# Optimization experiments

Measured on AMD Instinct MI355X. Metric: run time of the kernel, lower is better.

The kernel has to match this reference:

```python
import jax, jax.numpy as jnp
import numpy as np
import math

B, S, D, H = 2, 4096, 512, 8
HD = D // H

def setup_inputs() -> dict:
    key = jax.random.key(0)
    ks = jax.random.split(key, 12)
    s = 0.02
    return {
        "query": jax.random.normal(ks[0], (B, S, D), jnp.float32),
        "key": jax.random.normal(ks[1], (B, S, D), jnp.float32),
        "value": jax.random.normal(ks[2], (B, S, D), jnp.float32),
        "mask": jnp.ones((B, S, S), dtype=bool),
        "Wq": jax.random.normal(ks[3], (D, D), jnp.float32) * s,
        "bq": jnp.zeros((D,), jnp.float32),
        "Wk": jax.random.normal(ks[4], (D, D), jnp.float32) * s,
        "bk": jnp.zeros((D,), jnp.float32),
        "Wv": jax.random.normal(ks[5], (D, D), jnp.float32) * s,
        "bv": jnp.zeros((D,), jnp.float32),
        "Wo": jax.random.normal(ks[6], (D, D), jnp.float32) * s,
        "bo": jnp.zeros((D,), jnp.float32),
    }

def reference(query, key, value, mask, Wq, bq, Wk, bk, Wv, bv, Wo, bo):
    # projections (torch Linear: x @ W.T + b)
    q = query @ Wq.T + bq   # [B,S,D]
    k = key @ Wk.T + bk
    v = value @ Wv.T + bv
    # split heads -> [B,H,S,hd]
    q = q.reshape(B, S, H, HD).transpose(0, 2, 1, 3)
    k = k.reshape(B, S, H, HD).transpose(0, 2, 1, 3)
    v = v.reshape(B, S, H, HD).transpose(0, 2, 1, 3)
    score = jnp.einsum('bhqd,bhkd->bhqk', q, k) / math.sqrt(HD)
    score = jnp.where(mask[:, None, :, :], score, -jnp.inf)
    weight = jax.nn.softmax(score, axis=-1)
    out = jnp.einsum('bhqk,bhkd->bhqd', weight, v)
    out = out.transpose(0, 2, 1, 3).reshape(B, S, D)
    return out @ Wo.T + bo
```

## Files before the change

### kernel.cpp

```cpp
#include <hip/hip_runtime.h>


typedef short s16x8 __attribute__((ext_vector_type(8)));
typedef float f32x4 __attribute__((ext_vector_type(4)));
typedef float f32x16 __attribute__((ext_vector_type(16)));
typedef unsigned u32x4 __attribute__((ext_vector_type(4)));

#define MFMA_BF16_16(a, b, c) __builtin_amdgcn_mfma_f32_16x16x32_bf16((a), (b), (c), 0, 0, 0)
#define MFMA_BF16_32(a, b, c) __builtin_amdgcn_mfma_f32_32x32x16_bf16((a), (b), (c), 0, 0, 0)

#if __has_builtin(__builtin_amdgcn_exp2f)
#define EXP2F __builtin_amdgcn_exp2f
#else
#define EXP2F exp2f
#endif

__device__ __forceinline__ unsigned short f2bf(float f) {
  unsigned u = __float_as_uint(f);
  u += 0x7FFFu + ((u >> 16) & 1u);
  return (unsigned short)(u >> 16);
}

__device__ __forceinline__ float bf2f(unsigned short u) {
  return __uint_as_float((unsigned)u << 16);
}

__device__ __forceinline__ unsigned cvt_pk_bf16(float lo, float hi) {
  unsigned r;
  asm("v_cvt_pk_bf16_f32 %0, %1, %2" : "=v"(r) : "v"(lo), "v"(hi));
  return r;
}

__device__ __forceinline__ void pl_swap(unsigned& a, unsigned& b) {
#if __has_builtin(__builtin_amdgcn_permlane32_swap)
  auto r = __builtin_amdgcn_permlane32_swap(a, b, false, false);
  a = r[0];
  b = r[1];
#else
  asm volatile("v_permlane32_swap_b32 %0, %1" : "+v"(a), "+v"(b));
#endif
}

__device__ __forceinline__ float partner_sum(float x) {
  unsigned a = __float_as_uint(x), b = a;
  pl_swap(a, b);
  return __uint_as_float(a) + __uint_as_float(b);
}

__device__ __forceinline__ float exp_block(f32x16& sc) {
#pragma unroll
  for (int r = 0; r < 16; ++r) sc[r] = EXP2F(sc[r]);
  const float a = (sc[0] + sc[1]) + (sc[2] + sc[3]);
  const float b = (sc[4] + sc[5]) + (sc[6] + sc[7]);
  const float c = (sc[8] + sc[9]) + (sc[10] + sc[11]);
  const float d = (sc[12] + sc[13]) + (sc[14] + sc[15]);
  return (a + b) + (c + d);
}

__device__ __forceinline__ ushort4 cvt4(float4 v) {
  ushort4 b;
  b.x = f2bf(v.x); b.y = f2bf(v.y); b.z = f2bf(v.z); b.w = f2bf(v.w);
  return b;
}

__global__ __launch_bounds__(256, 3) void gemm_qkv(const float* __restrict__ Aq,
                                                   const float* __restrict__ Ak,
                                                   const float* __restrict__ Av,
                                                   const float* __restrict__ Wq,
                                                   const float* __restrict__ Wk,
                                                   const float* __restrict__ Wv,
                                                   const float* __restrict__ bq,
                                                   const float* __restrict__ bk,
                                                   const float* __restrict__ bv,
                                                   unsigned short* __restrict__ oq,
                                                   unsigned short* __restrict__ ok,
                                                   unsigned short* __restrict__ ov,
                                                   float qscale) {
  constexpr int KD = 512;
  __shared__ unsigned short As[128][72];
  __shared__ unsigned short Bs[128][72];

  const int bid = blockIdx.x;
  const int wg = (bid & 7) * 96 + (bid >> 3);
  const int n0 = (wg & 3) * 128;
  const int mseg = wg >> 2;
  const int seg = mseg >> 6;
  const int m0 = (mseg & 63) * 128;

  const float* A = (seg == 0) ? Aq : (seg == 1) ? Ak : Av;
  const float* W = (seg == 0) ? Wq : (seg == 1) ? Wk : Wv;
  const float* bias = (seg == 0) ? bq : (seg == 1) ? bk : bv;
  unsigned short* outb = (seg == 0) ? oq : (seg == 1) ? ok : ov;
  const float scale = (seg == 0) ? qscale : 1.0f;

  const int t = threadIdx.x;
  const int lane = t & 63;
  const int w = t >> 6;
  const int wr = w >> 1, wc = w & 1;
  const int x = lane & 15, g = lane >> 4;

  const f32x4 ZERO = {0.f, 0.f, 0.f, 0.f};
  f32x4 acc[4][4];
#pragma unroll
  for (int i = 0; i < 4; ++i)
#pragma unroll
    for (int j = 0; j < 4; ++j) acc[i][j] = ZERO;

  const int r0 = t >> 4, c4 = t & 15;

  float4 av[8];
#pragma unroll
  for (int i = 0; i < 8; ++i)
    av[i] = *(const float4*)(A + (size_t)(m0 + r0 + 16 * i) * KD + c4 * 4);

  for (int kt = 0; kt < KD / 64; ++kt) {
    const int k0 = kt * 64;
    if (kt) __syncthreads();
    float4 wtmp[8];
#pragma unroll
    for (int i = 0; i < 8; ++i)
      wtmp[i] = *(const float4*)(W + (size_t)(n0 + r0 + 16 * i) * KD + k0 + c4 * 4);
#pragma unroll
    for (int i = 0; i < 8; ++i)
      *(ushort4*)(&As[r0 + 16 * i][c4 * 4]) = cvt4(av[i]);
#pragma unroll
    for (int i = 0; i < 8; ++i)
      *(ushort4*)(&Bs[r0 + 16 * i][c4 * 4]) = cvt4(wtmp[i]);
    if (kt < 7) {
#pragma unroll
      for (int i = 0; i < 8; ++i)
        av[i] = *(const float4*)(A + (size_t)(m0 + r0 + 16 * i) * KD + k0 + 64 + c4 * 4);
    }
    __syncthreads();
#pragma unroll
    for (int ks = 0; ks < 2; ++ks) {
      s16x8 af[4], bfq[4];
#pragma unroll
      for (int mt = 0; mt < 4; ++mt)
        af[mt] = *(const s16x8*)(&As[wr * 64 + mt * 16 + x][ks * 32 + g * 8]);
#pragma unroll
      for (int nt = 0; nt < 4; ++nt)
        bfq[nt] = *(const s16x8*)(&Bs[wc * 64 + nt * 16 + x][ks * 32 + g * 8]);
#pragma unroll
      for (int mt = 0; mt < 4; ++mt)
#pragma unroll
        for (int nt = 0; nt < 4; ++nt)
          acc[mt][nt] = MFMA_BF16_16(af[mt], bfq[nt], acc[mt][nt]);
    }
  }

#pragma unroll
  for (int mt = 0; mt < 4; ++mt) {
#pragma unroll
    for (int nt = 0; nt < 4; ++nt) {
      const int n = n0 + wc * 64 + nt * 16 + x;
      const float bv2 = bias[n];
      const int h = n >> 6, hd = n & 63;
#pragma unroll
      for (int r = 0; r < 4; ++r) {
        const int m = m0 + wr * 64 + mt * 16 + g * 4 + r;
        const float val = (acc[mt][nt][r] + bv2) * scale;
        const int b = m >> 12, s = m & 4095;
        size_t off;
        if (seg < 2)
          off = ((size_t)(b * 8 + h) * 4096 + s) * 64 + hd;
        else
          off = ((size_t)(b * 8 + h) * 64 + hd) * 4096 + s;
        outb[off] = f2bf(val);
      }
    }
  }
}

__global__ __launch_bounds__(256, 3) void gemm_o(const unsigned short* __restrict__ o0,
                                                 const unsigned short* __restrict__ o1,
                                                 const float* __restrict__ l0,
                                                 const float* __restrict__ l1,
                                                 const float* __restrict__ W,
                                                 const float* __restrict__ bias,
                                                 float* __restrict__ out) {
  constexpr int KD = 512;
  __shared__ unsigned short As[64][72];
  __shared__ unsigned short Bs[128][72];

  const int bid = blockIdx.x;
  const int wg = (bid & 7) * 64 + (bid >> 3);
  const int n0 = (wg & 3) * 128;
  const int m0 = (wg >> 2) * 64;

  const int t = threadIdx.x;
  const int lane = t & 63;
  const int w = t >> 6;
  const int wr = w >> 1, wc = w & 1;
  const int x = lane & 15, g = lane >> 4;

  const f32x4 ZERO = {0.f, 0.f, 0.f, 0.f};
  f32x4 acc[2][4];
#pragma unroll
  for (int i = 0; i < 2; ++i)
#pragma unroll
    for (int j = 0; j < 4; ++j) acc[i][j] = ZERO;

  const int r0 = t >> 4, c4 = t & 15;

  int rowi[2], segi[2], bi[2], si[2];
  s16x8 pa[2], pb[2];
  float l0v[2], l1v[2];
#pragma unroll
  for (int i = 0; i < 2; ++i) {
    const int c = t + 256 * i;
    rowi[i] = c >> 3;
    segi[i] = c & 7;
    const int m = m0 + rowi[i];
    bi[i] = m >> 12;
    si[i] = m & 4095;
    const size_t ao = (size_t)m * 512 + segi[i] * 8;
    pa[i] = *(const s16x8*)(o0 + ao);
    pb[i] = *(const s16x8*)(o1 + ao);
    l0v[i] = l0[(size_t)(bi[i] * 8 + 0) * 4096 + si[i]];
    l1v[i] = l1[(size_t)(bi[i] * 8 + 0) * 4096 + si[i]];
  }

  for (int kt = 0; kt < KD / 64; ++kt) {
    const int k0 = kt * 64;
    if (kt) __syncthreads();
    float4 wtmp[8];
#pragma unroll
    for (int i = 0; i < 8; ++i)
      wtmp[i] = *(const float4*)(W + (size_t)(n0 + r0 + 16 * i) * KD + k0 + c4 * 4);
#pragma unroll
    for (int i = 0; i < 2; ++i) {
      const float inv = 1.0f / (l0v[i] + l1v[i]);
      const s16x8 A0 = pa[i], A1 = pb[i];
      unsigned q0_ = cvt_pk_bf16((bf2f(A0[0]) + bf2f(A1[0])) * inv,
                                 (bf2f(A0[1]) + bf2f(A1[1])) * inv);
      unsigned q1_ = cvt_pk_bf16((bf2f(A0[2]) + bf2f(A1[2])) * inv,
                                 (bf2f(A0[3]) + bf2f(A1[3])) * inv);
      unsigned q2_ = cvt_pk_bf16((bf2f(A0[4]) + bf2f(A1[4])) * inv,
                                 (bf2f(A0[5]) + bf2f(A1[5])) * inv);
      unsigned q3_ = cvt_pk_bf16((bf2f(A0[6]) + bf2f(A1[6])) * inv,
                                 (bf2f(A0[7]) + bf2f(A1[7])) * inv);
      u32x4 fu = {q0_, q1_, q2_, q3_};
      *(s16x8*)(&As[rowi[i]][segi[i] * 8]) = __builtin_bit_cast(s16x8, fu);
    }
#pragma unroll
    for (int i = 0; i < 8; ++i)
      *(ushort4*)(&Bs[r0 + 16 * i][c4 * 4]) = cvt4(wtmp[i]);
    if (kt < 7) {
      const int h = kt + 1;
#pragma unroll
      for (int i = 0; i < 2; ++i) {
        const size_t ao = (size_t)(m0 + rowi[i]) * 512 + h * 64 + segi[i] * 8;
        pa[i] = *(const s16x8*)(o0 + ao);
        pb[i] = *(const s16x8*)(o1 + ao);
        l0v[i] = l0[(size_t)(bi[i] * 8 + h) * 4096 + si[i]];
        l1v[i] = l1[(size_t)(bi[i] * 8 + h) * 4096 + si[i]];
      }
    }
    __syncthreads();
#pragma unroll
    for (int ks = 0; ks < 2; ++ks) {
      s16x8 af[2], bfq[4];
#pragma unroll
      for (int mt = 0; mt < 2; ++mt)
        af[mt] = *(const s16x8*)(&As[wr * 32 + mt * 16 + x][ks * 32 + g * 8]);
#pragma unroll
      for (int nt = 0; nt < 4; ++nt)
        bfq[nt] = *(const s16x8*)(&Bs[wc * 64 + nt * 16 + x][ks * 32 + g * 8]);
#pragma unroll
      for (int mt = 0; mt < 2; ++mt)
#pragma unroll
        for (int nt = 0; nt < 4; ++nt)
          acc[mt][nt] = MFMA_BF16_16(af[mt], bfq[nt], acc[mt][nt]);
    }
  }

#pragma unroll
  for (int mt = 0; mt < 2; ++mt) {
#pragma unroll
    for (int nt = 0; nt < 4; ++nt) {
      const int n = n0 + wc * 64 + nt * 16 + x;
      const float bv = bias[n];
#pragma unroll
      for (int r = 0; r < 4; ++r) {
        const int m = m0 + wr * 32 + mt * 16 + g * 4 + r;
        out[(size_t)m * 512 + n] = acc[mt][nt][r] + bv;
      }
    }
  }
}

__global__ __launch_bounds__(512, 2) void attn_fwd(const unsigned short* __restrict__ Qw,
                                                   const unsigned short* __restrict__ Kw,
                                                   const unsigned short* __restrict__ Vw,
                                                   unsigned short* __restrict__ Op,
                                                   float* __restrict__ Lp) {
  constexpr int S = 4096;
  constexpr int NP = 16;
  __shared__ unsigned short SM[8][64][72];

  const int t = threadIdx.x;
  const int lane = t & 63;
  const int w = t >> 6;
  const int q = lane & 31;
  const int hi = lane >> 5;

  const int bid = blockIdx.x;
  const int xcd = bid & 7;
  const int slot = bid >> 3;
  const int bh = xcd * 2 + (slot & 1);
  const int rest = slot >> 1;
  const int chunk = rest >> 4;
  const int qx = rest & 15;
  const int q0 = qx * 256 + w * 32;

  const unsigned short* Qb = Qw + (size_t)bh * S * 64;
  const unsigned short* Kb = Kw + (size_t)bh * S * 64 + (size_t)chunk * 2048 * 64;
  const unsigned short* Vb = Vw + (size_t)bh * 64 * S + chunk * 2048;

  s16x8 qf[4];
#pragma unroll
  for (int ks = 0; ks < 4; ++ks)
    qf[ks] = *(const s16x8*)(Qb + (size_t)(q0 + q) * 64 + ks * 16 + hi * 8);

  const f32x16 NEG8 = -8.0f;
  f32x16 ot0 = 0.f, ot1 = 0.f;
  float l_loc = 0.f;

  const int strow = t >> 3, stseg = t & 7;
  const unsigned short* kp = Kb + (size_t)strow * 64 + stseg * 8;
  const unsigned short* vp = Vb + (size_t)strow * S + stseg * 8;

  *(s16x8*)(&SM[0][strow][stseg * 8]) = *(const s16x8*)(kp);
  *(s16x8*)(&SM[1][strow][stseg * 8]) = *(const s16x8*)(kp + 4096);
  *(s16x8*)(&SM[4][strow][stseg * 8]) = *(const s16x8*)(vp);
  *(s16x8*)(&SM[5][strow][stseg * 8]) = *(const s16x8*)(vp + 64);
  s16x8 krA = *(const s16x8*)(kp + 2 * 4096);
  s16x8 krB = *(const s16x8*)(kp + 3 * 4096);
  s16x8 vrA = *(const s16x8*)(vp + 128);
  s16x8 vrB = *(const s16x8*)(vp + 192);
  __syncthreads();

  f32x16 sc0 = NEG8, sc1 = NEG8, sc2 = NEG8, sc3 = NEG8;

  __builtin_amdgcn_s_setprio(1);
#pragma unroll
  for (int ks = 0; ks < 4; ++ks) {
    const int col = ks * 16 + hi * 8;
    s16x8 a00 = *(const s16x8*)(&SM[0][q][col]);
    s16x8 a01 = *(const s16x8*)(&SM[0][32 + q][col]);
    s16x8 a10 = *(const s16x8*)(&SM[1][q][col]);
    s16x8 a11 = *(const s16x8*)(&SM[1][32 + q][col]);
    sc0 = MFMA_BF16_32(a00, qf[ks], sc0);
    sc1 = MFMA_BF16_32(a01, qf[ks], sc1);
    sc2 = MFMA_BF16_32(a10, qf[ks], sc2);
    sc3 = MFMA_BF16_32(a11, qf[ks], sc3);
  }
  __builtin_amdgcn_s_setprio(0);

  for (int p = 0; p < NP; ++p) {
    const int cb = (p & 1) * 2;
    const int nb = ((p + 1) & 1) * 2;

    if (p + 1 < NP) {
      *(s16x8*)(&SM[nb][strow][stseg * 8]) = krA;
      *(s16x8*)(&SM[nb + 1][strow][stseg * 8]) = krB;
      *(s16x8*)(&SM[4 + nb][strow][stseg * 8]) = vrA;
      *(s16x8*)(&SM[5 + nb][strow][stseg * 8]) = vrB;
    }
    if (p + 2 < NP) {
      krA = *(const s16x8*)(kp + (size_t)(2 * p + 4) * 4096);
      krB = *(const s16x8*)(kp + (size_t)(2 * p + 5) * 4096);
      vrA = *(const s16x8*)(vp + (2 * p + 4) * 64);
      vrB = *(const s16x8*)(vp + (2 * p + 5) * 64);
    }

    l_loc += exp_block(sc0);
    l_loc += exp_block(sc1);
    l_loc += exp_block(sc2);
    l_loc += exp_block(sc3);

#define PV_HALF(SC, VB, CBASE)                                                \
    _Pragma("unroll")                                                         \
    for (int cc = 0; cc < 2; ++cc) {                                          \
      const int b0 = cc * 8;                                                  \
      unsigned w0 = cvt_pk_bf16(SC[b0 + 0], SC[b0 + 1]);                      \
      unsigned w1 = cvt_pk_bf16(SC[b0 + 2], SC[b0 + 3]);                      \
      unsigned w2 = cvt_pk_bf16(SC[b0 + 4], SC[b0 + 5]);                      \
      unsigned w3 = cvt_pk_bf16(SC[b0 + 6], SC[b0 + 7]);                      \
      pl_swap(w0, w2);                                                        \
      pl_swap(w1, w3);                                                        \
      u32x4 fu = {w0, w1, w2, w3};                                            \
      const s16x8 pf = __builtin_bit_cast(s16x8, fu);                         \
      const int col = (CBASE + cc) * 16 + hi * 8;                             \
      __builtin_amdgcn_s_setprio(1);                                          \
      {                                                                       \
        s16x8 a0 = *(const s16x8*)(&SM[VB][q][col]);                          \
        s16x8 a1 = *(const s16x8*)(&SM[VB][32 + q][col]);                     \
        ot0 = MFMA_BF16_32(a0, pf, ot0);                                      \
        ot1 = MFMA_BF16_32(a1, pf, ot1);                                      \
      }                                                                       \
      __builtin_amdgcn_s_setprio(0);                                          \
    }

    PV_HALF(sc0, 4 + cb, 0)
    PV_HALF(sc1, 4 + cb, 2)
    PV_HALF(sc2, 5 + cb, 0)
    PV_HALF(sc3, 5 + cb, 2)
#undef PV_HALF

    __syncthreads();

    if (p + 1 < NP) {
      sc0 = NEG8; sc1 = NEG8; sc2 = NEG8; sc3 = NEG8;
      __builtin_amdgcn_s_setprio(1);
#pragma unroll
      for (int ks = 0; ks < 4; ++ks) {
        const int col = ks * 16 + hi * 8;
        s16x8 a00 = *(const s16x8*)(&SM[nb][q][col]);
        s16x8 a01 = *(const s16x8*)(&SM[nb][32 + q][col]);
        s16x8 a10 = *(const s16x8*)(&SM[nb + 1][q][col]);
        s16x8 a11 = *(const s16x8*)(&SM[nb + 1][32 + q][col]);
        sc0 = MFMA_BF16_32(a00, qf[ks], sc0);
        sc1 = MFMA_BF16_32(a01, qf[ks], sc1);
        sc2 = MFMA_BF16_32(a10, qf[ks], sc2);
        sc3 = MFMA_BF16_32(a11, qf[ks], sc3);
      }
      __builtin_amdgcn_s_setprio(0);
    }
  }

  unsigned short* EP = &SM[0][0][0];
  const int erow = w * 32 + q;
#pragma unroll
  for (int c = 0; c < 4; ++c) {
    const int d = 8 * c + 4 * hi;
    *(unsigned*)(EP + erow * 72 + d) = cvt_pk_bf16(ot0[4 * c + 0], ot0[4 * c + 1]);
    *(unsigned*)(EP + erow * 72 + d + 2) = cvt_pk_bf16(ot0[4 * c + 2], ot0[4 * c + 3]);
    *(unsigned*)(EP + erow * 72 + 32 + d) = cvt_pk_bf16(ot1[4 * c + 0], ot1[4 * c + 1]);
    *(unsigned*)(EP + erow * 72 + 32 + d + 2) = cvt_pk_bf16(ot1[4 * c + 2], ot1[4 * c + 3]);
  }
  const float lf = partner_sum(l_loc);
  if (hi == 0)
    Lp[((size_t)chunk * 16 + bh) * 4096 + q0 + q] = lf;

  const int bb = bh >> 3, h = bh & 7;
  unsigned short* Ob = Op + (size_t)chunk * 8192 * 512;
#pragma unroll
  for (int i = 0; i < 4; ++i) {
    const int r = i * 8 + (lane >> 3), sg = lane & 7;
    s16x8 vrow = *(const s16x8*)(EP + (w * 32 + r) * 72 + sg * 8);
    *(s16x8*)(Ob + ((size_t)(bb * 4096 + q0 + r)) * 512 + h * 64 + sg * 8) = vrow;
  }
}

extern "C" void kernel_launch(void* const* d_in, const int* in_sizes, int n_in,
                              void* d_out, int out_size, void* d_ws, size_t ws_size,
                              hipStream_t stream) {
  const float* query = (const float*)d_in[0];
  const float* keyin = (const float*)d_in[1];
  const float* value = (const float*)d_in[2];
  const float* Wq = (const float*)d_in[4];
  const float* bq = (const float*)d_in[5];
  const float* Wk = (const float*)d_in[6];
  const float* bk = (const float*)d_in[7];
  const float* Wv = (const float*)d_in[8];
  const float* bv = (const float*)d_in[9];
  const float* Wo = (const float*)d_in[10];
  const float* bo = (const float*)d_in[11];
  float* out = (float*)d_out;

  unsigned short* qws = (unsigned short*)d_ws;
  unsigned short* kws = qws + (size_t)8192 * 512;
  unsigned short* vws = kws + (size_t)8192 * 512;
  unsigned short* opart = vws + (size_t)8192 * 512;
  float* lpart = (float*)(opart + (size_t)2 * 8192 * 512);

  const float qscale = 0.125f * 1.44269504f;
  gemm_qkv<<<768, 256, 0, stream>>>(query, keyin, value, Wq, Wk, Wv,
                                    bq, bk, bv, qws, kws, vws, qscale);
  attn_fwd<<<512, 512, 0, stream>>>(qws, kws, vws, opart, lpart);
  gemm_o<<<512, 256, 0, stream>>>(opart, opart + (size_t)8192 * 512,
                                  lpart, lpart + (size_t)16 * 4096,
                                  Wo, bo, out);
}
```

Measured before the change: 137.9 us.

## Restructure attention to 4 waves with 64 query rows each and 64-key tiles

The attention kernel drops from 8 to 4 waves per block, and each wave now owns 64 query rows in two 32-row groups. Each K/V fragment read from shared memory therefore feeds twice as many MFMAs, which cuts LDS traffic per FLOP. The key loop now steps through 32 tiles of 64 keys with a smaller double buffer, and the cross-iteration QK prefetch is gone. Separately, the GEMM kernels replace the software bf16 rounding with the packed hardware convert. The cost is higher register pressure (more accumulators and Q fragments), and fewer waves are left to hide latency.

```diff
diff --git a/kernel.cpp b/kernel.cpp
--- a/kernel.cpp
+++ b/kernel.cpp
@@ -5,6 +5,7 @@
 typedef float f32x4 __attribute__((ext_vector_type(4)));
 typedef float f32x16 __attribute__((ext_vector_type(16)));
 typedef unsigned u32x4 __attribute__((ext_vector_type(4)));
+typedef unsigned u32x2 __attribute__((ext_vector_type(2)));
 
 #define MFMA_BF16_16(a, b, c) __builtin_amdgcn_mfma_f32_16x16x32_bf16((a), (b), (c), 0, 0, 0)
 #define MFMA_BF16_32(a, b, c) __builtin_amdgcn_mfma_f32_32x32x16_bf16((a), (b), (c), 0, 0, 0)
@@ -15,12 +16,6 @@
 #define EXP2F exp2f
 #endif
 
-__device__ __forceinline__ unsigned short f2bf(float f) {
-  unsigned u = __float_as_uint(f);
-  u += 0x7FFFu + ((u >> 16) & 1u);
-  return (unsigned short)(u >> 16);
-}
-
 __device__ __forceinline__ float bf2f(unsigned short u) {
   return __uint_as_float((unsigned)u << 16);
 }
@@ -28,6 +23,11 @@
 __device__ __forceinline__ unsigned cvt_pk_bf16(float lo, float hi) {
   unsigned r;
   asm("v_cvt_pk_bf16_f32 %0, %1, %2" : "=v"(r) : "v"(lo), "v"(hi));
+  return r;
+}
+
+__device__ __forceinline__ u32x2 cvt4pk(float4 v) {
+  u32x2 r = {cvt_pk_bf16(v.x, v.y), cvt_pk_bf16(v.z, v.w)};
   return r;
 }
 
@@ -57,10 +57,16 @@
   return (a + b) + (c + d);
 }
 
-__device__ __forceinline__ ushort4 cvt4(float4 v) {
-  ushort4 b;
-  b.x = f2bf(v.x); b.y = f2bf(v.y); b.z = f2bf(v.z); b.w = f2bf(v.w);
-  return b;
+__device__ __forceinline__ s16x8 make_pf(float s0, float s1, float s2, float s3,
+                                         float s4, float s5, float s6, float s7) {
+  unsigned w0 = cvt_pk_bf16(s0, s1);
+  unsigned w1 = cvt_pk_bf16(s2, s3);
+  unsigned w2 = cvt_pk_bf16(s4, s5);
+  unsigned w3 = cvt_pk_bf16(s6, s7);
+  pl_swap(w0, w2);
+  pl_swap(w1, w3);
+  u32x4 fu = {w0, w1, w2, w3};
+  return __builtin_bit_cast(s16x8, fu);
 }
 
 __global__ __launch_bounds__(256, 3) void gemm_qkv(const float* __restrict__ Aq,
@@ -122,10 +128,10 @@
       wtmp[i] = *(const float4*)(W + (size_t)(n0 + r0 + 16 * i) * KD + k0 + c4 * 4);
 #pragma unroll
     for (int i = 0; i < 8; ++i)
-      *(ushort4*)(&As[r0 + 16 * i][c4 * 4]) = cvt4(av[i]);
+      *(u32x2*)(&As[r0 + 16 * i][c4 * 4]) = cvt4pk(av[i]);
 #pragma unroll
     for (int i = 0; i < 8; ++i)
-      *(ushort4*)(&Bs[r0 + 16 * i][c4 * 4]) = cvt4(wtmp[i]);
+      *(u32x2*)(&Bs[r0 + 16 * i][c4 * 4]) = cvt4pk(wtmp[i]);
     if (kt < 7) {
 #pragma unroll
       for (int i = 0; i < 8; ++i)
@@ -166,7 +172,8 @@
           off = ((size_t)(b * 8 + h) * 4096 + s) * 64 + hd;
         else
           off = ((size_t)(b * 8 + h) * 64 + hd) * 4096 + s;
-        outb[off] = f2bf(val);
+        const unsigned short bf = (unsigned short)(cvt_pk_bf16(val, val) & 0xffffu);
+        outb[off] = bf;
       }
     }
   }
@@ -245,7 +252,7 @@
     }
 #pragma unroll
     for (int i = 0; i < 8; ++i)
-      *(ushort4*)(&Bs[r0 + 16 * i][c4 * 4]) = cvt4(wtmp[i]);
+      *(u32x2*)(&Bs[r0 + 16 * i][c4 * 4]) = cvt4pk(wtmp[i]);
     if (kt < 7) {
       const int h = kt + 1;
 #pragma unroll
@@ -290,14 +297,14 @@
   }
 }
 
-__global__ __launch_bounds__(512, 2) void attn_fwd(const unsigned short* __restrict__ Qw,
+__global__ __launch_bounds__(256, 2) void attn_fwd(const unsigned short* __restrict__ Qw,
                                                    const unsigned short* __restrict__ Kw,
                                                    const unsigned short* __restrict__ Vw,
                                                    unsigned short* __restrict__ Op,
                                                    float* __restrict__ Lp) {
   constexpr int S = 4096;
-  constexpr int NP = 16;
-  __shared__ unsigned short SM[8][64][72];
+  constexpr int NT = 32;
+  __shared__ unsigned short SM[4][64][72];
 
   const int t = threadIdx.x;
   const int lane = t & 63;
@@ -312,144 +319,146 @@
   const int rest = slot >> 1;
   const int chunk = rest >> 4;
   const int qx = rest & 15;
-  const int q0 = qx * 256 + w * 32;
+  const int q0 = qx * 256 + w * 64;
 
   const unsigned short* Qb = Qw + (size_t)bh * S * 64;
   const unsigned short* Kb = Kw + (size_t)bh * S * 64 + (size_t)chunk * 2048 * 64;
   const unsigned short* Vb = Vw + (size_t)bh * 64 * S + chunk * 2048;
 
-  s16x8 qf[4];
-#pragma unroll
-  for (int ks = 0; ks < 4; ++ks)
-    qf[ks] = *(const s16x8*)(Qb + (size_t)(q0 + q) * 64 + ks * 16 + hi * 8);
+  s16x8 qf[2][4];
+#pragma unroll
+  for (int qg = 0; qg < 2; ++qg)
+#pragma unroll
+    for (int ks = 0; ks < 4; ++ks)
+      qf[qg][ks] = *(const s16x8*)(Qb + (size_t)(q0 + qg * 32 + q) * 64 + ks * 16 + hi * 8);
 
   const f32x16 NEG8 = -8.0f;
-  f32x16 ot0 = 0.f, ot1 = 0.f;
-  float l_loc = 0.f;
-
-  const int strow = t >> 3, stseg = t & 7;
-  const unsigned short* kp = Kb + (size_t)strow * 64 + stseg * 8;
-  const unsigned short* vp = Vb + (size_t)strow * S + stseg * 8;
-
-  *(s16x8*)(&SM[0][strow][stseg * 8]) = *(const s16x8*)(kp);
-  *(s16x8*)(&SM[1][strow][stseg * 8]) = *(const s16x8*)(kp + 4096);
-  *(s16x8*)(&SM[4][strow][stseg * 8]) = *(const s16x8*)(vp);
-  *(s16x8*)(&SM[5][strow][stseg * 8]) = *(const s16x8*)(vp + 64);
-  s16x8 krA = *(const s16x8*)(kp + 2 * 4096);
-  s16x8 krB = *(const s16x8*)(kp + 3 * 4096);
-  s16x8 vrA = *(const s16x8*)(vp + 128);
-  s16x8 vrB = *(const s16x8*)(vp + 192);
+  f32x16 ot00 = 0.f, ot01 = 0.f, ot10 = 0.f, ot11 = 0.f;
+  float l_0 = 0.f, l_1 = 0.f;
+
+  int lrow[2], lseg[2];
+  const unsigned short* kpp[2];
+  const unsigned short* vpp[2];
+#pragma unroll
+  for (int i = 0; i < 2; ++i) {
+    const int c = t + 256 * i;
+    lrow[i] = c >> 3;
+    lseg[i] = c & 7;
+    kpp[i] = Kb + (size_t)lrow[i] * 64 + lseg[i] * 8;
+    vpp[i] = Vb + (size_t)lrow[i] * S + lseg[i] * 8;
+  }
+
+  s16x8 kreg[2], vreg[2];
+#pragma unroll
+  for (int i = 0; i < 2; ++i) {
+    *(s16x8*)(&SM[0][lrow[i]][lseg[i] * 8]) = *(const s16x8*)(kpp[i]);
+    *(s16x8*)(&SM[2][lrow[i]][lseg[i] * 8]) = *(const s16x8*)(vpp[i]);
+  }
+#pragma unroll
+  for (int i = 0; i < 2; ++i) {
+    kreg[i] = *(const s16x8*)(kpp[i] + 4096);
+    vreg[i] = *(const s16x8*)(vpp[i] + 64);
+  }
   __syncthreads();
 
-  f32x16 sc0 = NEG8, sc1 = NEG8, sc2 = NEG8, sc3 = NEG8;
-
-  __builtin_amdgcn_s_setprio(1);
-#pragma unroll
-  for (int ks = 0; ks < 4; ++ks) {
-    const int col = ks * 16 + hi * 8;
-    s16x8 a00 = *(const s16x8*)(&SM[0][q][col]);
-    s16x8 a01 = *(const s16x8*)(&SM[0][32 + q][col]);
-    s16x8 a10 = *(const s16x8*)(&SM[1][q][col]);
-    s16x8 a11 = *(const s16x8*)(&SM[1][32 + q][col]);
-    sc0 = MFMA_BF16_32(a00, qf[ks], sc0);
-    sc1 = MFMA_BF16_32(a01, qf[ks], sc1);
-    sc2 = MFMA_BF16_32(a10, qf[ks], sc2);
-    sc3 = MFMA_BF16_32(a11, qf[ks], sc3);
-  }
-  __builtin_amdgcn_s_setprio(0);
-
-  for (int p = 0; p < NP; ++p) {
-    const int cb = (p & 1) * 2;
-    const int nb = ((p + 1) & 1) * 2;
-
-    if (p + 1 < NP) {
-      *(s16x8*)(&SM[nb][strow][stseg * 8]) = krA;
-      *(s16x8*)(&SM[nb + 1][strow][stseg * 8]) = krB;
-      *(s16x8*)(&SM[4 + nb][strow][stseg * 8]) = vrA;
-      *(s16x8*)(&SM[5 + nb][strow][stseg * 8]) = vrB;
-    }
-    if (p + 2 < NP) {
-      krA = *(const s16x8*)(kp + (size_t)(2 * p + 4) * 4096);
-      krB = *(const s16x8*)(kp + (size_t)(2 * p + 5) * 4096);
-      vrA = *(const s16x8*)(vp + (2 * p + 4) * 64);
-      vrB = *(const s16x8*)(vp + (2 * p + 5) * 64);
-    }
-
-    l_loc += exp_block(sc0);
-    l_loc += exp_block(sc1);
-    l_loc += exp_block(sc2);
-    l_loc += exp_block(sc3);
-
-#define PV_HALF(SC, VB, CBASE)                                                \
-    _Pragma("unroll")                                                         \
-    for (int cc = 0; cc < 2; ++cc) {                                          \
-      const int b0 = cc * 8;                                                  \
-      unsigned w0 = cvt_pk_bf16(SC[b0 + 0], SC[b0 + 1]);                      \
-      unsigned w1 = cvt_pk_bf16(SC[b0 + 2], SC[b0 + 3]);                      \
-      unsigned w2 = cvt_pk_bf16(SC[b0 + 4], SC[b0 + 5]);                      \
-      unsigned w3 = cvt_pk_bf16(SC[b0 + 6], SC[b0 + 7]);                      \
-      pl_swap(w0, w2);                                                        \
-      pl_swap(w1, w3);                                                        \
-      u32x4 fu = {w0, w1, w2, w3};                                            \
-      const s16x8 pf = __builtin_bit_cast(s16x8, fu);                         \
-      const int col = (CBASE + cc) * 16 + hi * 8;                             \
-      __builtin_amdgcn_s_setprio(1);                                          \
-      {                                                                       \
-        s16x8 a0 = *(const s16x8*)(&SM[VB][q][col]);                          \
-        s16x8 a1 = *(const s16x8*)(&SM[VB][32 + q][col]);                     \
-        ot0 = MFMA_BF16_32(a0, pf, ot0);                                      \
-        ot1 = MFMA_BF16_32(a1, pf, ot1);                                      \
-      }                                                                       \
-      __builtin_amdgcn_s_setprio(0);                                          \
-    }
-
-    PV_HALF(sc0, 4 + cb, 0)
-    PV_HALF(sc1, 4 + cb, 2)
-    PV_HALF(sc2, 5 + cb, 0)
-    PV_HALF(sc3, 5 + cb, 2)
-#undef PV_HALF
+  for (int kt = 0; kt < NT; ++kt) {
+    const int cb = kt & 1;
+    const int nb = cb ^ 1;
+
+    if (kt + 1 < NT) {
+#pragma unroll
+      for (int i = 0; i < 2; ++i) {
+        *(s16x8*)(&SM[nb][lrow[i]][lseg[i] * 8]) = kreg[i];
+        *(s16x8*)(&SM[2 + nb][lrow[i]][lseg[i] * 8]) = vreg[i];
+      }
+    }
+    if (kt + 2 < NT) {
+#pragma unroll
+      for (int i = 0; i < 2; ++i) {
+        kreg[i] = *(const s16x8*)(kpp[i] + (size_t)(kt + 2) * 4096);
+        vreg[i] = *(const s16x8*)(vpp[i] + (kt + 2) * 64);
+      }
+    }
+
+    f32x16 sc00 = NEG8, sc01 = NEG8, sc10 = NEG8, sc11 = NEG8;
+    __builtin_amdgcn_s_setprio(1);
+#pragma unroll
+    for (int ks = 0; ks < 4; ++ks) {
+      const int col = ks * 16 + hi * 8;
+      s16x8 a0 = *(const s16x8*)(&SM[cb][q][col]);
+      s16x8 a1 = *(const s16x8*)(&SM[cb][32 + q][col]);
+      sc00 = MFMA_BF16_32(a0, qf[0][ks], sc00);
+      sc01 = MFMA_BF16_32(a0, qf[1][ks], sc01);
+      sc10 = MFMA_BF16_32(a1, qf[0][ks], sc10);
+      sc11 = MFMA_BF16_32(a1, qf[1][ks], sc11);
+    }
+    __builtin_amdgcn_s_setprio(0);
+
+    l_0 += exp_block(sc00);
+    l_0 += exp_block(sc10);
+    l_1 += exp_block(sc01);
+    l_1 += exp_block(sc11);
+
+#pragma unroll
+    for (int c = 0; c < 4; ++c) {
+      s16x8 pf0, pf1;
+      if (c == 0) {
+        pf0 = make_pf(sc00[0], sc00[1], sc00[2], sc00[3], sc00[4], sc00[5], sc00[6], sc00[7]);
+        pf1 = make_pf(sc01[0], sc01[1], sc01[2], sc01[3], sc01[4], sc01[5], sc01[6], sc01[7]);
+      } else if (c == 1) {
+        pf0 = make_pf(sc00[8], sc00[9], sc00[10], sc00[11], sc00[12], sc00[13], sc00[14], sc00[15]);
+        pf1 = make_pf(sc01[8], sc01[9], sc01[10], sc01[11], sc01[12], sc01[13], sc01[14], sc01[15]);
+      } else if (c == 2) {
+        pf0 = make_pf(sc10[0], sc10[1], sc10[2], sc10[3], sc10[4], sc10[5], sc10[6], sc10[7]);
+        pf1 = make_pf(sc11[0], sc11[1], sc11[2], sc11[3], sc11[4], sc11[5], sc11[6], sc11[7]);
+      } else {
+        pf0 = make_pf(sc10[8], sc10[9], sc10[10], sc10[11], sc10[12], sc10[13], sc10[14], sc10[15]);
+        pf1 = make_pf(sc11[8], sc11[9], sc11[10], sc11[11], sc11[12], sc11[13], sc11[14], sc11[15]);
+      }
+      const int col = c * 16 + hi * 8;
+      __builtin_amdgcn_s_setprio(1);
+      {
+        s16x8 va = *(const s16x8*)(&SM[2 + cb][q][col]);
+        s16x8 vb = *(const s16x8*)(&SM[2 + cb][32 + q][col]);
+        ot00 = MFMA_BF16_32(va, pf0, ot00);
+        ot01 = MFMA_BF16_32(va, pf1, ot01);
+        ot10 = MFMA_BF16_32(vb, pf0, ot10);
+        ot11 = MFMA_BF16_32(vb, pf1, ot11);
+      }
+      __builtin_amdgcn_s_setprio(0);
+    }
 
     __syncthreads();
-
-    if (p + 1 < NP) {
-      sc0 = NEG8; sc1 = NEG8; sc2 = NEG8; sc3 = NEG8;
-      __builtin_amdgcn_s_setprio(1);
-#pragma unroll
-      for (int ks = 0; ks < 4; ++ks) {
-        const int col = ks * 16 + hi * 8;
-        s16x8 a00 = *(const s16x8*)(&SM[nb][q][col]);
-        s16x8 a01 = *(const s16x8*)(&SM[nb][32 + q][col]);
-        s16x8 a10 = *(const s16x8*)(&SM[nb + 1][q][col]);
-        s16x8 a11 = *(const s16x8*)(&SM[nb + 1][32 + q][col]);
-        sc0 = MFMA_BF16_32(a00, qf[ks], sc0);
-        sc1 = MFMA_BF16_32(a01, qf[ks], sc1);
-        sc2 = MFMA_BF16_32(a10, qf[ks], sc2);
-        sc3 = MFMA_BF16_32(a11, qf[ks], sc3);
-      }
-      __builtin_amdgcn_s_setprio(0);
-    }
   }
 
   unsigned short* EP = &SM[0][0][0];
-  const int erow = w * 32 + q;
-#pragma unroll
-  for (int c = 0; c < 4; ++c) {
-    const int d = 8 * c + 4 * hi;
-    *(unsigned*)(EP + erow * 72 + d) = cvt_pk_bf16(ot0[4 * c + 0], ot0[4 * c + 1]);
-    *(unsigned*)(EP + erow * 72 + d + 2) = cvt_pk_bf16(ot0[4 * c + 2], ot0[4 * c + 3]);
-    *(unsigned*)(EP + erow * 72 + 32 + d) = cvt_pk_bf16(ot1[4 * c + 0], ot1[4 * c + 1]);
-    *(unsigned*)(EP + erow * 72 + 32 + d + 2) = cvt_pk_bf16(ot1[4 * c + 2], ot1[4 * c + 3]);
-  }
-  const float lf = partner_sum(l_loc);
-  if (hi == 0)
-    Lp[((size_t)chunk * 16 + bh) * 4096 + q0 + q] = lf;
+#pragma unroll
+  for (int qg = 0; qg < 2; ++qg) {
+    const int erow = w * 64 + qg * 32 + q;
+    const f32x16& o0r = (qg == 0) ? ot00 : ot01;
+    const f32x16& o1r = (qg == 0) ? ot10 : ot11;
+#pragma unroll
+    for (int c = 0; c < 4; ++c) {
+      const int d = 8 * c + 4 * hi;
+      *(unsigned*)(EP + erow * 72 + d) = cvt_pk_bf16(o0r[4 * c + 0], o0r[4 * c + 1]);
+      *(unsigned*)(EP + erow * 72 + d + 2) = cvt_pk_bf16(o0r[4 * c + 2], o0r[4 * c + 3]);
+      *(unsigned*)(EP + erow * 72 + 32 + d) = cvt_pk_bf16(o1r[4 * c + 0], o1r[4 * c + 1]);
+      *(unsigned*)(EP + erow * 72 + 32 + d + 2) = cvt_pk_bf16(o1r[4 * c + 2], o1r[4 * c + 3]);
+    }
+  }
+  const float lf0 = partner_sum(l_0);
+  const float lf1 = partner_sum(l_1);
+  if (hi == 0) {
+    Lp[((size_t)chunk * 16 + bh) * 4096 + q0 + q] = lf0;
+    Lp[((size_t)chunk * 16 + bh) * 4096 + q0 + 32 + q] = lf1;
+  }
 
   const int bb = bh >> 3, h = bh & 7;
   unsigned short* Ob = Op + (size_t)chunk * 8192 * 512;
 #pragma unroll
-  for (int i = 0; i < 4; ++i) {
+  for (int i = 0; i < 8; ++i) {
     const int r = i * 8 + (lane >> 3), sg = lane & 7;
-    s16x8 vrow = *(const s16x8*)(EP + (w * 32 + r) * 72 + sg * 8);
+    s16x8 vrow = *(const s16x8*)(EP + (w * 64 + r) * 72 + sg * 8);
     *(s16x8*)(Ob + ((size_t)(bb * 4096 + q0 + r)) * 512 + h * 64 + sg * 8) = vrow;
   }
 }
@@ -479,7 +488,7 @@
   const float qscale = 0.125f * 1.44269504f;
   gemm_qkv<<<768, 256, 0, stream>>>(query, keyin, value, Wq, Wk, Wv,
                                     bq, bk, bv, qws, kws, vws, qscale);
-  attn_fwd<<<512, 512, 0, stream>>>(qws, kws, vws, opart, lpart);
+  attn_fwd<<<512, 256, 0, stream>>>(qws, kws, vws, opart, lpart);
   gemm_o<<<512, 256, 0, stream>>>(opart, opart + (size_t)8192 * 512,
                                   lpart, lpart + (size_t)16 * 4096,
                                   Wo, bo, out);
```

After: 129.5 us, median of 3. -6.1%, faster.
